# Optimization experiments

Hardware: AMD Instinct MI355X
Metric: run time of the kernel (lower is better)

The kernel has to match this reference:

```python
import jax, jax.numpy as jnp
import numpy as np

B, S, HID = 1, 2048, 2048
NH = 16
D_NOPE, D_ROPE, D_V = 128, 64, 128
D_QK = D_NOPE + D_ROPE            # 192
KV_R = 512                        # kv_lora_rank
EPS = 1e-6
SCALING = D_QK ** -0.5
NEG = -1e9


def rms_norm(x, w):
    xf = x.astype(jnp.float32)
    var = jnp.mean(xf * xf, axis=-1, keepdims=True)
    return w * (xf * jax.lax.rsqrt(var + EPS)).astype(x.dtype)


def rotate_half(x):
    x1, x2 = jnp.split(x, 2, axis=-1)
    return jnp.concatenate([-x2, x1], axis=-1)


def deinterleave(x):
    # torch: view(..., d//2, 2).transpose(-1, -2).reshape(..., d)
    # => [x0, x2, x4, ..., x1, x3, x5, ...]
    return jnp.concatenate([x[..., 0::2], x[..., 1::2]], axis=-1)


def setup_inputs() -> dict:
    key = jax.random.key(0)
    ks = jax.random.split(key, 6)
    hidden_states = jax.random.normal(ks[0], (B, S, HID), jnp.float32)
    # rotary cos/sin over qk_rope_head_dim
    inv_freq = 1.0 / (10000.0 ** (np.arange(0, D_ROPE, 2, dtype=np.float32) / D_ROPE))
    freqs = np.outer(np.arange(S, dtype=np.float32), inv_freq)   # [S, D_ROPE/2]
    emb = np.concatenate([freqs, freqs], axis=-1)                # [S, D_ROPE]
    cos = jnp.asarray(np.cos(emb), jnp.float32)[None]            # [1, S, D_ROPE]
    sin = jnp.asarray(np.sin(emb), jnp.float32)[None]
    # additive causal mask [1, 1, S, S]
    causal = np.where(np.tril(np.ones((S, S), dtype=bool)), 0.0, NEG).astype(np.float32)
    attention_mask = jnp.asarray(causal)[None, None]
    sc = lambda k, shp: jax.random.normal(k, shp, jnp.float32) * (shp[-1] ** -0.5)
    q_proj_w = sc(ks[1], (NH * D_QK, HID))
    kv_a_proj_w = sc(ks[2], (KV_R + D_ROPE, HID))
    kv_a_ln_w = jnp.ones((KV_R,), jnp.float32)
    kv_b_proj_w = sc(ks[3], (NH * (D_NOPE + D_V), KV_R))
    o_proj_w = sc(ks[4], (HID, NH * D_V))
    return dict(hidden_states=hidden_states, cos=cos, sin=sin,
                attention_mask=attention_mask, q_proj_w=q_proj_w,
                kv_a_proj_w=kv_a_proj_w, kv_a_ln_w=kv_a_ln_w,
                kv_b_proj_w=kv_b_proj_w, o_proj_w=o_proj_w)


def reference(hidden_states, cos, sin, attention_mask,
              q_proj_w, kv_a_proj_w, kv_a_ln_w, kv_b_proj_w, o_proj_w):
    b, s, _ = hidden_states.shape
    # Q projection -> [b, NH, s, D_QK]
    q = (hidden_states @ q_proj_w.T).reshape(b, s, NH, D_QK).transpose(0, 2, 1, 3)
    q_pass, q_rot = q[..., :D_NOPE], q[..., D_NOPE:]
    # compressed KV + shared rope key
    ckv = hidden_states @ kv_a_proj_w.T                           # [b, s, KV_R + D_ROPE]
    k_pass_c, k_rot = ckv[..., :KV_R], ckv[..., KV_R:]
    kv = (rms_norm(k_pass_c, kv_a_ln_w) @ kv_b_proj_w.T)
    kv = kv.reshape(b, s, NH, D_NOPE + D_V).transpose(0, 2, 1, 3)  # [b, NH, s, .]
    k_pass, value_states = kv[..., :D_NOPE], kv[..., D_NOPE:]
    k_rot = k_rot.reshape(b, 1, s, D_ROPE)
    # interleaved RoPE (rope_interleave=True)
    q_rot = deinterleave(q_rot)
    k_rot = deinterleave(k_rot)
    c = cos[:, None]  # [1, 1, s, D_ROPE]
    sn = sin[:, None]
    q_rot = q_rot * c + rotate_half(q_rot) * sn
    k_rot = k_rot * c + rotate_half(k_rot) * sn
    k_rot = jnp.broadcast_to(k_rot, (b, NH, s, D_ROPE))
    query_states = jnp.concatenate([q_pass, q_rot], axis=-1)      # [b, NH, s, D_QK]
    key_states = jnp.concatenate([k_pass, k_rot], axis=-1)
    # eager attention (num_key_value_groups == 1)
    scores = jnp.einsum('bhqd,bhkd->bhqk', query_states, key_states) * SCALING
    scores = scores + attention_mask[:, :, :, :s]
    attn = jax.nn.softmax(scores.astype(jnp.float32), axis=-1).astype(query_states.dtype)
    attn_out = jnp.einsum('bhqk,bhkd->bhqd', attn, value_states)  # [b, NH, s, D_V]
    attn_out = attn_out.transpose(0, 2, 1, 3).reshape(b, s, NH * D_V)
    return attn_out @ o_proj_w.T
```

## Files before the change

kernel.cpp:

```cpp
#include <hip/hip_runtime.h>
#include <hip/hip_bf16.h>
#include <stdint.h>
#include <stddef.h>

#define S_LEN 2048
#define HID_DIM 2048
#define NH 16
#define D_QK 192
#define D_NOPE 128
#define D_ROPE 64
#define D_V 128
#define KV_R 512
#define CKV_N (KV_R + D_ROPE)
#define KVB_N (NH * (D_NOPE + D_V))
#define QN (NH * D_QK)
#define CAT_N (QN + CKV_N)
#define SCALING 0.07216878364870322f

typedef __attribute__((ext_vector_type(8))) short short8;
typedef __attribute__((ext_vector_type(4))) short short4v;
typedef __attribute__((ext_vector_type(4))) float f32x4;

__device__ __forceinline__ short f2bf_bits(float f) {
  unsigned u = __float_as_uint(f);
  unsigned r = (u + 0x7fffu + ((u >> 16) & 1u)) >> 16;
  return (short)(r & 0xffffu);
}
__device__ __forceinline__ float bf2f(short b) {
  return __uint_as_float(((unsigned)(unsigned short)b) << 16);
}

__device__ __forceinline__ f32x4 mfma_bf16(short8 a, short8 b, f32x4 c) {
  return __builtin_amdgcn_mfma_f32_16x16x32_bf16(a, b, c, 0, 0, 0);
}

__global__ __launch_bounds__(256)
void cvt5_k(const float* __restrict__ s0, short* __restrict__ d0, int c0,
            const float* __restrict__ s1, short* __restrict__ d1, int c1,
            const float* __restrict__ s2, short* __restrict__ d2, int c2,
            const float* __restrict__ s3, short* __restrict__ d3, int c3,
            const float* __restrict__ s4, short* __restrict__ d4, int c4) {
  const int i = blockIdx.x * 256 + threadIdx.x;
  const float* s; short* d; int base;
  if      (i < c0) { s = s0; d = d0; base = 0;  }
  else if (i < c1) { s = s1; d = d1; base = c0; }
  else if (i < c2) { s = s2; d = d2; base = c1; }
  else if (i < c3) { s = s3; d = d3; base = c2; }
  else if (i < c4) { s = s4; d = d4; base = c3; }
  else return;
  const int j = i - base;
  const float4 v = ((const float4*)s)[j];
  short4v o;
  o.x = f2bf_bits(v.x); o.y = f2bf_bits(v.y);
  o.z = f2bf_bits(v.z); o.w = f2bf_bits(v.w);
  ((short4v*)d)[j] = o;
}

template <bool OUTF32>
__global__ __launch_bounds__(256, 3)
void gemm_bt(const short* __restrict__ A, const short* __restrict__ B,
             void* __restrict__ Cv, int M, int N, int K) {
  __shared__ short sA[2][128 * 32];
  __shared__ short sB[2][128 * 32];
  const int tid  = threadIdx.x;
  const int wave = tid >> 6;
  const int lane = tid & 63;
  const int bm = blockIdx.y * 128;
  const int bn = blockIdx.x * 128;
  const int wr = wave >> 1, wc = wave & 1;
  const int fr = lane & 15, fk = (lane >> 4) * 8;
  const int srow = lane >> 2;
  const int scol = (lane & 3) * 8;

  f32x4 acc[4][4];
  for (int i = 0; i < 4; ++i)
    for (int j = 0; j < 4; ++j)
      for (int r = 0; r < 4; ++r) acc[i][j][r] = 0.f;

  for (int k0 = 0; k0 < K; k0 += 64) {
    __syncthreads();
#pragma unroll
    for (int cc = 0; cc < 2; ++cc) {
      const int c = wave * 2 + cc;
      const int ar = bm + c * 16 + srow;
      int br = bn + c * 16 + srow; if (br > N - 1) br = N - 1;
#pragma unroll
      for (int kh = 0; kh < 2; ++kh) {
        __builtin_amdgcn_global_load_lds(
            (const __attribute__((address_space(1))) void*)(A + (size_t)ar * K + k0 + kh * 32 + scol),
            (__attribute__((address_space(3))) void*)(sA[kh] + c * 512), 16, 0, 0);
        __builtin_amdgcn_global_load_lds(
            (const __attribute__((address_space(1))) void*)(B + (size_t)br * K + k0 + kh * 32 + scol),
            (__attribute__((address_space(3))) void*)(sB[kh] + c * 512), 16, 0, 0);
      }
    }
    __syncthreads();
#pragma unroll
    for (int kh = 0; kh < 2; ++kh) {
      short8 af[4], bfr[4];
#pragma unroll
      for (int i = 0; i < 4; ++i)
        af[i] = *(const short8*)(sA[kh] + (wr * 64 + i * 16 + fr) * 32 + fk);
#pragma unroll
      for (int j = 0; j < 4; ++j)
        bfr[j] = *(const short8*)(sB[kh] + (wc * 64 + j * 16 + fr) * 32 + fk);
#pragma unroll
      for (int i = 0; i < 4; ++i)
#pragma unroll
        for (int j = 0; j < 4; ++j)
          acc[i][j] = mfma_bf16(af[i], bfr[j], acc[i][j]);
    }
  }

  const int cr = (lane >> 4) * 4, ccol = lane & 15;
#pragma unroll
  for (int i = 0; i < 4; ++i)
#pragma unroll
    for (int j = 0; j < 4; ++j) {
      const int col = bn + wc * 64 + j * 16 + ccol;
      if (col < N) {
#pragma unroll
        for (int r = 0; r < 4; ++r) {
          const int row = bm + wr * 64 + i * 16 + cr + r;
          if (OUTF32)
            ((float*)Cv)[(size_t)row * N + col] = acc[i][j][r];
          else
            ((short*)Cv)[(size_t)row * N + col] = f2bf_bits(acc[i][j][r]);
        }
      }
    }
}

__global__ __launch_bounds__(256)
void rmsnorm_k(const short* __restrict__ qckv, const float* __restrict__ w,
               short* __restrict__ out) {
  const int s = blockIdx.x, t = threadIdx.x;
  const short* x = qckv + (size_t)s * CAT_N + QN;
  float v0 = bf2f(x[2 * t]), v1 = bf2f(x[2 * t + 1]);
  float ss = v0 * v0 + v1 * v1;
#pragma unroll
  for (int off = 1; off < 64; off <<= 1) ss += __shfl_xor(ss, off, 64);
  __shared__ float red[4];
  if ((t & 63) == 0) red[t >> 6] = ss;
  __syncthreads();
  const float tot = red[0] + red[1] + red[2] + red[3];
  const float sc = rsqrtf(tot * (1.0f / 512.0f) + 1e-6f);
  out[(size_t)s * KV_R + 2 * t]     = f2bf_bits(v0 * sc * w[2 * t]);
  out[(size_t)s * KV_R + 2 * t + 1] = f2bf_bits(v1 * sc * w[2 * t + 1]);
}

__global__ __launch_bounds__(256)
void prep_k(const short* __restrict__ qckv, const short* __restrict__ kvb,
            const float* __restrict__ cosb, const float* __restrict__ sinb,
            short* __restrict__ Qs, short* __restrict__ Ks) {
  const int s = blockIdx.x, t = threadIdx.x;
  const short* qrow = qckv + (size_t)s * CAT_N;
  __shared__ float cs[32], sn[32];
  __shared__ short krs[64];
  if (t < 32) {
    const float c  = cosb[(size_t)s * 64 + t];
    const float si = sinb[(size_t)s * 64 + t];
    cs[t] = c; sn[t] = si;
    const float e0 = bf2f(qrow[QN + KV_R + 2 * t]);
    const float e1 = bf2f(qrow[QN + KV_R + 2 * t + 1]);
    krs[t]      = f2bf_bits(e0 * c - e1 * si);
    krs[t + 32] = f2bf_bits(e1 * c + e0 * si);
  }
  __syncthreads();
  const int h = t >> 4, i = t & 15;
  *(short8*)(Qs + ((size_t)h * S_LEN + s) * D_QK + i * 8) =
      *(const short8*)(qrow + h * D_QK + i * 8);
  *(short8*)(Ks + ((size_t)h * S_LEN + s) * D_QK + i * 8) =
      *(const short8*)(kvb + (size_t)s * KVB_N + h * 256 + i * 8);
#pragma unroll
  for (int p = 0; p < 2; ++p) {
    const int ii = i * 2 + p;
    const float e0 = bf2f(qrow[h * D_QK + 128 + 2 * ii]);
    const float e1 = bf2f(qrow[h * D_QK + 128 + 2 * ii + 1]);
    Qs[((size_t)h * S_LEN + s) * D_QK + 128 + ii] = f2bf_bits(e0 * cs[ii] - e1 * sn[ii]);
    Qs[((size_t)h * S_LEN + s) * D_QK + 160 + ii] = f2bf_bits(e1 * cs[ii] + e0 * sn[ii]);
  }
#pragma unroll
  for (int p = 0; p < 4; ++p) {
    const int idx = t * 4 + p;
    const int hh = idx >> 6, ii = idx & 63;
    Ks[((size_t)hh * S_LEN + s) * D_QK + 128 + ii] = krs[ii];
  }
}

__global__ __launch_bounds__(256)
void vtr_k(const short* __restrict__ kvb, short* __restrict__ Vt) {
  const int st = blockIdx.x, dt = blockIdx.y, h = blockIdx.z;
  __shared__ short sT[64][72];
  const int id = threadIdx.x;
#pragma unroll
  for (int p = 0; p < 2; ++p) {
    const int q = id + p * 256;
    const int row = q >> 3, c8 = q & 7;
    *(short8*)(&sT[row][c8 * 8]) =
        *(const short8*)(kvb + (size_t)(st * 64 + row) * KVB_N + h * 256 + 128 + dt * 64 + c8 * 8);
  }
  __syncthreads();
#pragma unroll
  for (int p = 0; p < 2; ++p) {
    const int q = id + p * 256;
    const int drow = q >> 3, c8 = q & 7;
    short8 o;
#pragma unroll
    for (int j = 0; j < 8; ++j) o[j] = sT[c8 * 8 + j][drow];
    *(short8*)(Vt + ((size_t)h * D_V + dt * 64 + drow) * S_LEN + st * 64 + c8 * 8) = o;
  }
}

__global__ __launch_bounds__(256, 2)
void flash_k(const short* __restrict__ Qs, const short* __restrict__ Ks,
             const short* __restrict__ Vt, short* __restrict__ Oc) {
  __shared__ short sK[64 * 200];
  __shared__ short sVt[128 * 72];
  __shared__ short P_lds[4][16 * 72];
  const int tid = threadIdx.x;
  const int wv = tid >> 6;
  const int lane = tid & 63;
  const int blk = blockIdx.x;
  const int h = ((blk & 7) << 1) | ((blk >> 3) & 1);
  const int qb = 31 - (blk >> 4);
  const int q0 = qb * 64 + wv * 16;
  const int fr = lane & 15, g = lane >> 4;

  const short* Qh = Qs + (size_t)h * S_LEN * D_QK;
  const short* Kh = Ks + (size_t)h * S_LEN * D_QK;
  const short* Vh = Vt + (size_t)h * D_V * S_LEN;

  int rowK[6], c8K[6], rowV[4], c8V[4];
#pragma unroll
  for (int p = 0; p < 6; ++p) {
    const int id = tid + p * 256;
    rowK[p] = id / 24; c8K[p] = id % 24;
  }
#pragma unroll
  for (int p = 0; p < 4; ++p) {
    const int id = tid + p * 256;
    rowV[p] = id >> 3; c8V[p] = id & 7;
  }

  short8 qa[6];
#pragma unroll
  for (int c = 0; c < 6; ++c)
    qa[c] = *(const short8*)(Qh + (size_t)(q0 + fr) * D_QK + c * 32 + g * 8);

  f32x4 o[8];
  for (int f = 0; f < 8; ++f)
    for (int r = 0; r < 4; ++r) o[f][r] = 0.f;
  float m_i[4] = {-1e30f, -1e30f, -1e30f, -1e30f};
  float l_i[4] = {0.f, 0.f, 0.f, 0.f};

  short8 kc[6], vc[4];
#pragma unroll
  for (int p = 0; p < 6; ++p)
    kc[p] = *(const short8*)(Kh + (size_t)rowK[p] * D_QK + c8K[p] * 8);
#pragma unroll
  for (int p = 0; p < 4; ++p)
    vc[p] = *(const short8*)(Vh + (size_t)rowV[p] * S_LEN + c8V[p] * 8);

  short* pl = &P_lds[wv][0];
  const int jn = qb + 1;
  for (int jt = 0; jt < jn; ++jt) {
    const int j0 = jt << 6;
    __syncthreads();
#pragma unroll
    for (int p = 0; p < 6; ++p)
      *(short8*)(sK + rowK[p] * 200 + c8K[p] * 8) = kc[p];
#pragma unroll
    for (int p = 0; p < 4; ++p)
      *(short8*)(sVt + rowV[p] * 72 + c8V[p] * 8) = vc[p];
    __syncthreads();
    if (jt + 1 < jn) {
      const int j1 = (jt + 1) << 6;
#pragma unroll
      for (int p = 0; p < 6; ++p)
        kc[p] = *(const short8*)(Kh + (size_t)(j1 + rowK[p]) * D_QK + c8K[p] * 8);
#pragma unroll
      for (int p = 0; p < 4; ++p)
        vc[p] = *(const short8*)(Vh + (size_t)rowV[p] * S_LEN + j1 + c8V[p] * 8);
    }

    f32x4 sc[4];
#pragma unroll
    for (int t = 0; t < 4; ++t)
      for (int r = 0; r < 4; ++r) sc[t][r] = -1e30f;
#pragma unroll
    for (int t = 0; t < 4; ++t) {
      if (j0 + t * 16 <= q0 + 15) {
        f32x4 a;
        for (int r = 0; r < 4; ++r) a[r] = 0.f;
        const short* kr = sK + (t * 16 + fr) * 200 + g * 8;
#pragma unroll
        for (int c = 0; c < 6; ++c)
          a = mfma_bf16(qa[c], *(const short8*)(kr + c * 32), a);
        sc[t] = a;
      }
    }
    float tm[4];
#pragma unroll
    for (int r = 0; r < 4; ++r) {
      const int row = q0 + g * 4 + r;
      float mx = -1e30f;
#pragma unroll
      for (int t = 0; t < 4; ++t) {
        const float v = (j0 + t * 16 + fr <= row) ? sc[t][r] * SCALING : -1e30f;
        sc[t][r] = v;
        mx = fmaxf(mx, v);
      }
      tm[r] = mx;
    }
#pragma unroll
    for (int off = 1; off < 16; off <<= 1)
#pragma unroll
      for (int r = 0; r < 4; ++r)
        tm[r] = fmaxf(tm[r], __shfl_xor(tm[r], off, 16));
    float ps[4];
#pragma unroll
    for (int r = 0; r < 4; ++r) {
      const float mnew = fmaxf(m_i[r], tm[r]);
      const float alpha = __expf(m_i[r] - mnew);
      m_i[r] = mnew;
      l_i[r] *= alpha;
      float s = 0.f;
#pragma unroll
      for (int t = 0; t < 4; ++t) {
        const float p = __expf(sc[t][r] - mnew);
        sc[t][r] = p;
        s += p;
      }
      ps[r] = s;
#pragma unroll
      for (int f = 0; f < 8; ++f) o[f][r] *= alpha;
    }
#pragma unroll
    for (int off = 1; off < 16; off <<= 1)
#pragma unroll
      for (int r = 0; r < 4; ++r)
        ps[r] += __shfl_xor(ps[r], off, 16);
#pragma unroll
    for (int r = 0; r < 4; ++r) l_i[r] += ps[r];

#pragma unroll
    for (int r = 0; r < 4; ++r)
#pragma unroll
      for (int t = 0; t < 4; ++t)
        pl[(g * 4 + r) * 72 + t * 16 + fr] = f2bf_bits(sc[t][r]);
    __builtin_amdgcn_fence(__ATOMIC_ACQ_REL, "wavefront");
    const short8 pa0 = *(const short8*)(pl + fr * 72 + g * 8);
    const short8 pa1 = *(const short8*)(pl + fr * 72 + 32 + g * 8);

#pragma unroll
    for (int f = 0; f < 8; ++f) {
      const short* vr = sVt + (f * 16 + fr) * 72 + g * 8;
      const short8 vb0 = *(const short8*)(vr);
      const short8 vb1 = *(const short8*)(vr + 32);
      o[f] = mfma_bf16(pa1, vb1, mfma_bf16(pa0, vb0, o[f]));
    }
  }

#pragma unroll
  for (int r = 0; r < 4; ++r) {
    const float inv = 1.0f / l_i[r];
    const int row = q0 + g * 4 + r;
#pragma unroll
    for (int f = 0; f < 8; ++f)
      Oc[(size_t)row * (NH * D_V) + h * D_V + f * 16 + fr] = f2bf_bits(o[f][r] * inv);
  }
}

extern "C" void kernel_launch(void* const* d_in, const int* in_sizes, int n_in,
                              void* d_out, int out_size, void* d_ws, size_t ws_size,
                              hipStream_t stream) {
  const float* hidden = (const float*)d_in[0];
  const float* cosb   = (const float*)d_in[1];
  const float* sinb   = (const float*)d_in[2];
  const float* q_w    = (const float*)d_in[4];
  const float* kva_w  = (const float*)d_in[5];
  const float* ln_w   = (const float*)d_in[6];
  const float* kvb_w  = (const float*)d_in[7];
  const float* o_w    = (const float*)d_in[8];
  float* out = (float*)d_out;

  char* ws = (char*)d_ws;
  size_t off = 0;
  auto alloc = [&](size_t elems) {
    short* p = (short*)(ws + off);
    off += ((elems * 2 + 255) & ~(size_t)255);
    return p;
  };
  short* hid_b   = alloc((size_t)S_LEN * HID_DIM);
  short* qkva_wb = alloc((size_t)CAT_N * HID_DIM);
  short* kvb_wb  = alloc((size_t)KVB_N * KV_R);
  short* o_wb    = alloc((size_t)HID_DIM * NH * D_V);
  short* qckv    = alloc((size_t)S_LEN * CAT_N);
  short* ckvn    = alloc((size_t)S_LEN * KV_R);
  short* kvb     = alloc((size_t)S_LEN * KVB_N);
  short* Qs      = alloc((size_t)NH * S_LEN * D_QK);
  short* Ks      = alloc((size_t)NH * S_LEN * D_QK);
  short* Vt      = alloc((size_t)NH * D_V * S_LEN);
  short* Oc      = alloc((size_t)S_LEN * NH * D_V);

  dim3 blk(256);
  const int n0 = (S_LEN * HID_DIM) / 4;
  const int n1 = (QN * HID_DIM) / 4;
  const int n2 = (CKV_N * HID_DIM) / 4;
  const int n3 = (KVB_N * KV_R) / 4;
  const int n4e = (HID_DIM * NH * D_V) / 4;
  const int c0 = n0, c1 = c0 + n1, c2 = c1 + n2, c3 = c2 + n3, c4 = c3 + n4e;
  cvt5_k<<<dim3((c4 + 255) / 256), blk, 0, stream>>>(
      hidden, hid_b, c0,
      q_w, qkva_wb, c1,
      kva_w, qkva_wb + (size_t)QN * HID_DIM, c2,
      kvb_w, kvb_wb, c3,
      o_w, o_wb, c4);

  gemm_bt<false><<<dim3((CAT_N + 127) / 128, S_LEN / 128), blk, 0, stream>>>(
      hid_b, qkva_wb, qckv, S_LEN, CAT_N, HID_DIM);
  rmsnorm_k<<<dim3(S_LEN), blk, 0, stream>>>(qckv, ln_w, ckvn);
  gemm_bt<false><<<dim3(KVB_N / 128, S_LEN / 128), blk, 0, stream>>>(
      ckvn, kvb_wb, kvb, S_LEN, KVB_N, KV_R);
  prep_k<<<dim3(S_LEN), blk, 0, stream>>>(qckv, kvb, cosb, sinb, Qs, Ks);
  vtr_k<<<dim3(S_LEN / 64, D_V / 64, NH), blk, 0, stream>>>(kvb, Vt);
  flash_k<<<dim3(NH * 128 / 4), blk, 0, stream>>>(Qs, Ks, Vt, Oc);
  gemm_bt<true><<<dim3(HID_DIM / 128, S_LEN / 128), blk, 0, stream>>>(
      Oc, o_wb, out, S_LEN, HID_DIM, NH * D_V);
}
```

Measured before the change: 312.9 us.

## Read K and V fragments directly from global memory in flash attention

Drops the LDS staging of K and V tiles, along with the block-wide barriers and register prefetch, in the flash attention kernel. Each wave now loads its MFMA operands for K and transposed V straight from global memory, relying on L1/L2 caching because the four waves of a block share the same tiles. This removes two __syncthreads per iteration and the LDS traffic, and frees LDS for occupancy. The cost is four times the global/cache load traffic, uncoalesced 16-byte row loads, and more load latency exposed without the software prefetch.

Result: slower. 447.9 us (+43.1%).

```diff
diff --git a/kernel.cpp b/kernel.cpp
--- a/kernel.cpp
+++ b/kernel.cpp
@@ -215,8 +215,6 @@
 __global__ __launch_bounds__(256, 2)
 void flash_k(const short* __restrict__ Qs, const short* __restrict__ Ks,
              const short* __restrict__ Vt, short* __restrict__ Oc) {
-  __shared__ short sK[64 * 200];
-  __shared__ short sVt[128 * 72];
   __shared__ short P_lds[4][16 * 72];
   const int tid = threadIdx.x;
   const int wv = tid >> 6;
@@ -231,18 +229,6 @@
   const short* Kh = Ks + (size_t)h * S_LEN * D_QK;
   const short* Vh = Vt + (size_t)h * D_V * S_LEN;
 
-  int rowK[6], c8K[6], rowV[4], c8V[4];
-#pragma unroll
-  for (int p = 0; p < 6; ++p) {
-    const int id = tid + p * 256;
-    rowK[p] = id / 24; c8K[p] = id % 24;
-  }
-#pragma unroll
-  for (int p = 0; p < 4; ++p) {
-    const int id = tid + p * 256;
-    rowV[p] = id >> 3; c8V[p] = id & 7;
-  }
-
   short8 qa[6];
 #pragma unroll
   for (int c = 0; c < 6; ++c)
@@ -254,35 +240,10 @@
   float m_i[4] = {-1e30f, -1e30f, -1e30f, -1e30f};
   float l_i[4] = {0.f, 0.f, 0.f, 0.f};
 
-  short8 kc[6], vc[4];
-#pragma unroll
-  for (int p = 0; p < 6; ++p)
-    kc[p] = *(const short8*)(Kh + (size_t)rowK[p] * D_QK + c8K[p] * 8);
-#pragma unroll
-  for (int p = 0; p < 4; ++p)
-    vc[p] = *(const short8*)(Vh + (size_t)rowV[p] * S_LEN + c8V[p] * 8);
-
   short* pl = &P_lds[wv][0];
   const int jn = qb + 1;
   for (int jt = 0; jt < jn; ++jt) {
     const int j0 = jt << 6;
-    __syncthreads();
-#pragma unroll
-    for (int p = 0; p < 6; ++p)
-      *(short8*)(sK + rowK[p] * 200 + c8K[p] * 8) = kc[p];
-#pragma unroll
-    for (int p = 0; p < 4; ++p)
-      *(short8*)(sVt + rowV[p] * 72 + c8V[p] * 8) = vc[p];
-    __syncthreads();
-    if (jt + 1 < jn) {
-      const int j1 = (jt + 1) << 6;
-#pragma unroll
-      for (int p = 0; p < 6; ++p)
-        kc[p] = *(const short8*)(Kh + (size_t)(j1 + rowK[p]) * D_QK + c8K[p] * 8);
-#pragma unroll
-      for (int p = 0; p < 4; ++p)
-        vc[p] = *(const short8*)(Vh + (size_t)rowV[p] * S_LEN + j1 + c8V[p] * 8);
-    }
 
     f32x4 sc[4];
 #pragma unroll
@@ -293,13 +254,22 @@
       if (j0 + t * 16 <= q0 + 15) {
         f32x4 a;
         for (int r = 0; r < 4; ++r) a[r] = 0.f;
-        const short* kr = sK + (t * 16 + fr) * 200 + g * 8;
+        const short* kr = Kh + (size_t)(j0 + t * 16 + fr) * D_QK + g * 8;
 #pragma unroll
         for (int c = 0; c < 6; ++c)
           a = mfma_bf16(qa[c], *(const short8*)(kr + c * 32), a);
         sc[t] = a;
       }
     }
+
+    short8 vb0a[8], vb1a[8];
+#pragma unroll
+    for (int f = 0; f < 8; ++f) {
+      const short* vr = Vh + (size_t)(f * 16 + fr) * S_LEN + j0 + g * 8;
+      vb0a[f] = *(const short8*)(vr);
+      vb1a[f] = *(const short8*)(vr + 32);
+    }
+
     float tm[4];
 #pragma unroll
     for (int r = 0; r < 4; ++r) {
@@ -354,12 +324,8 @@
     const short8 pa1 = *(const short8*)(pl + fr * 72 + 32 + g * 8);
 
 #pragma unroll
-    for (int f = 0; f < 8; ++f) {
-      const short* vr = sVt + (f * 16 + fr) * 72 + g * 8;
-      const short8 vb0 = *(const short8*)(vr);
-      const short8 vb1 = *(const short8*)(vr + 32);
-      o[f] = mfma_bf16(pa1, vb1, mfma_bf16(pa0, vb0, o[f]));
-    }
+    for (int f = 0; f < 8; ++f)
+      o[f] = mfma_bf16(pa1, vb1a[f], mfma_bf16(pa0, vb0a[f], o[f]));
   }
 
 #pragma unroll
```
